# Optimization experiments

Measured on AMD Instinct MI355X. Metric: run time of the kernel, lower is better.

The kernel has to match this reference:

```python
import jax, jax.numpy as jnp
import numpy as np

FEATURE_DIM = 768
LAMBDA_REG = 0.01
NUM_ITERS = 5
LR = 0.1
SIGMA = 2.0
MARGIN = 1.0
BN_EPS = 1e-5


def setup_inputs() -> dict:
    key = jax.random.key(0)
    ks = jax.random.split(key, 10)
    B, D = 32, FEATURE_DIM
    search_features = jax.random.normal(ks[0], (B, D, 32, 32), dtype=jnp.float32)
    target_features = jax.random.normal(ks[1], (B, D, 16, 16), dtype=jnp.float32)
    target_mask = jax.random.uniform(ks[2], (B, 1, 16, 16), dtype=jnp.float32)
    conv_w = jax.random.normal(ks[3], (D, D), dtype=jnp.float32) * (1.0 / np.sqrt(D))
    conv_b = jax.random.normal(ks[4], (D,), dtype=jnp.float32) * 0.01
    bn_gamma = jnp.ones((D,), dtype=jnp.float32)
    bn_beta = jnp.zeros((D,), dtype=jnp.float32)
    bn_mean = jax.random.normal(ks[5], (D,), dtype=jnp.float32) * 0.01
    bn_var = jax.random.uniform(ks[6], (D,), dtype=jnp.float32, minval=0.5, maxval=1.5)
    filter_init = jax.random.normal(ks[7], (1, D, 1, 1), dtype=jnp.float32) * 0.01
    return {
        "search_features": search_features,
        "target_features": target_features,
        "target_mask": target_mask,
        "conv_w": conv_w,
        "conv_b": conv_b,
        "bn_gamma": bn_gamma,
        "bn_beta": bn_beta,
        "bn_mean": bn_mean,
        "bn_var": bn_var,
        "filter_init": filter_init,
    }


def _proj(x, conv_w, conv_b, bn_gamma, bn_beta, bn_mean, bn_var):
    # 1x1 conv == channel-wise GEMM, then BatchNorm (eval mode, running stats)
    y = jnp.einsum('bdhw,ed->behw', x, conv_w) + conv_b[None, :, None, None]
    inv_std = bn_gamma / jnp.sqrt(bn_var + BN_EPS)
    return (y - bn_mean[None, :, None, None]) * inv_std[None, :, None, None] + bn_beta[None, :, None, None]


def _gaussian_label(mask):
    B, _, H, W = mask.shape
    yy, xx = jnp.meshgrid(jnp.arange(H, dtype=jnp.float32), jnp.arange(W, dtype=jnp.float32), indexing='ij')
    yy = yy[None, None]  # (1,1,H,W)
    xx = xx[None, None]
    msum = jnp.clip(mask.sum(axis=(2, 3), keepdims=True), 1.0)
    cy = (mask * yy).sum(axis=(2, 3), keepdims=True) / msum
    cx = (mask * xx).sum(axis=(2, 3), keepdims=True) / msum
    return jnp.exp(-((xx - cx) ** 2 + (yy - cy) ** 2) / (2.0 * SIGMA ** 2))


def reference(search_features, target_features, target_mask, conv_w, conv_b,
              bn_gamma, bn_beta, bn_mean, bn_var, filter_init):
    sp = _proj(search_features, conv_w, conv_b, bn_gamma, bn_beta, bn_mean, bn_var)
    tp = _proj(target_features, conv_w, conv_b, bn_gamma, bn_beta, bn_mean, bn_var)
    B = tp.shape[0]
    label = _gaussian_label(target_mask)  # (B,1,H',W')
    f = jnp.broadcast_to(filter_init, (B,) + filter_init.shape[1:])  # (B,D,1,1)
    for _ in range(NUM_ITERS):
        response = (tp * f).sum(axis=1, keepdims=True)  # (B,1,H',W')
        loss = jnp.maximum(MARGIN - response * label, 0.0)
        grad = jnp.where(loss > 0, -label * target_mask, 0.0)
        grad = grad.mean(axis=(2, 3), keepdims=True)  # (B,1,1,1), broadcasts over D
        f = f - LR * (grad + LAMBDA_REG * f)
    return (sp * f).sum(axis=1, keepdims=True)  # (B,1,H,W)
```

## Files before the change

### kernel.cpp

```cpp
#include <hip/hip_runtime.h>
#include <math.h>

#define DD   768
#define BB   32
#define NTP  256
#define NSP  1024
#define NT   (BB*NTP)
#define NS   (BB*NSP)
#define ECH  48
#define CHE  (DD/ECH)

#define OFF_UP  0
#define OFF_VP  (OFF_UP + ECH*DD)
#define OFF_U   (OFF_VP + ECH*DD)
#define OFF_V   (OFF_U + DD)
#define OFF_K   (OFF_V + DD)
#define OFF_C5  (OFF_K + 16)
#define OFF_TR0 (OFF_C5 + 48)
#define OFF_TS0 (OFF_TR0 + NT)

#define A5 0.99500999000499900f

__global__ void k_prep(const float* __restrict__ w, const float* __restrict__ cb,
                       const float* __restrict__ gamma, const float* __restrict__ beta,
                       const float* __restrict__ mean, const float* __restrict__ var,
                       const float* __restrict__ fi, float* __restrict__ ws) {
    int bx = blockIdx.x;
    int t = threadIdx.x;
    if (bx < ECH) {
        __shared__ float wu[CHE], wv[CHE];
        if (t < CHE) {
            int e = bx * CHE + t;
            float inv = gamma[e] / sqrtf(var[e] + 1e-5f);
            wv[t] = inv;
            wu[t] = inv * fi[e];
        }
        __syncthreads();
        if (t < 192) {
            const float4* w4 = (const float4*)w;
            float4 Ru = {0,0,0,0}, Rv = {0,0,0,0};
            #pragma unroll
            for (int j = 0; j < CHE; ++j) {
                float4 x = w4[(size_t)(bx * CHE + j) * 192 + t];
                float a = wu[j], b = wv[j];
                Ru.x += x.x * a; Ru.y += x.y * a; Ru.z += x.z * a; Ru.w += x.w * a;
                Rv.x += x.x * b; Rv.y += x.y * b; Rv.z += x.z * b; Rv.w += x.w * b;
            }
            *(float4*)(ws + OFF_UP + bx * DD + t * 4) = Ru;
            *(float4*)(ws + OFF_VP + bx * DD + t * 4) = Rv;
        }
    } else {
        __shared__ float r1[256], r2[256];
        float a1 = 0.f, a2 = 0.f;
        for (int e = t; e < DD; e += 256) {
            float inv = gamma[e] / sqrtf(var[e] + 1e-5f);
            float x = (cb[e] - mean[e]) * inv + beta[e];
            a1 += x * fi[e];
            a2 += x;
        }
        r1[t] = a1; r2[t] = a2;
        __syncthreads();
        for (int s = 128; s > 0; s >>= 1) {
            if (t < s) { r1[t] += r1[t + s]; r2[t] += r2[t + s]; }
            __syncthreads();
        }
        if (t == 0) { ws[OFF_K] = r1[0]; ws[OFF_K + 1] = r2[0]; }
    }
}

__global__ void k_prep2(float* __restrict__ ws) {
    int bx = blockIdx.x;
    int d = (bx % 3) * 256 + threadIdx.x;
    int isV = bx / 3;
    int srcOff = isV ? OFF_VP : OFF_UP;
    int dstOff = isV ? OFF_V : OFF_U;
    float a = 0.f;
    #pragma unroll 8
    for (int ec = 0; ec < ECH; ++ec) a += ws[srcOff + ec * DD + d];
    ws[dstOff + d] = a;
}

__global__ __launch_bounds__(256) void k_dots_t(const float* __restrict__ tf,
                                                float* __restrict__ ws) {
    int t = threadIdx.x;
    int px = t & 15, sub = t >> 4;
    __shared__ float su[DD], sv[DD];
    for (int i = t; i < DD; i += 256) { su[i] = ws[OFF_U + i]; sv[i] = ws[OFF_V + i]; }
    __syncthreads();
    int pf = blockIdx.x * 16 + px;
    int b = pf >> 6;
    const float4* base = (const float4*)tf + ((size_t)b * DD + sub * 48) * (NTP/4) + (pf & 63);
    const int STR = NTP / 4;
    float4 accR = {0,0,0,0}, accS = {0,0,0,0};
    float4 buf[8];
    #pragma unroll
    for (int k = 0; k < 8; ++k) buf[k] = base[(size_t)k * STR];
    #pragma unroll
    for (int g = 1; g < 6; ++g) {
        float4 nxt[8];
        #pragma unroll
        for (int k = 0; k < 8; ++k) nxt[k] = base[(size_t)(g * 8 + k) * STR];
        #pragma unroll
        for (int k = 0; k < 8; ++k) {
            int ch = sub * 48 + (g - 1) * 8 + k;
            float u = su[ch], v = sv[ch];
            accR.x += buf[k].x * u; accR.y += buf[k].y * u; accR.z += buf[k].z * u; accR.w += buf[k].w * u;
            accS.x += buf[k].x * v; accS.y += buf[k].y * v; accS.z += buf[k].z * v; accS.w += buf[k].w * v;
            buf[k] = nxt[k];
        }
    }
    #pragma unroll
    for (int k = 0; k < 8; ++k) {
        int ch = sub * 48 + 40 + k;
        float u = su[ch], v = sv[ch];
        accR.x += buf[k].x * u; accR.y += buf[k].y * u; accR.z += buf[k].z * u; accR.w += buf[k].w * u;
        accS.x += buf[k].x * v; accS.y += buf[k].y * v; accS.z += buf[k].z * v; accS.w += buf[k].w * v;
    }
    __shared__ float4 redR[16][16], redS[16][16];
    redR[sub][px] = accR; redS[sub][px] = accS;
    __syncthreads();
    for (int s = 8; s > 0; s >>= 1) {
        if (sub < s) {
            float4 a = redR[sub + s][px], m = redR[sub][px];
            m.x += a.x; m.y += a.y; m.z += a.z; m.w += a.w; redR[sub][px] = m;
            float4 c = redS[sub + s][px], n = redS[sub][px];
            n.x += c.x; n.y += c.y; n.z += c.z; n.w += c.w; redS[sub][px] = n;
        }
        __syncthreads();
    }
    if (sub == 0) {
        ((float4*)(ws + OFF_TR0))[pf] = redR[0][px];
        ((float4*)(ws + OFF_TS0))[pf] = redS[0][px];
    }
}

__global__ void k_filter(const float* __restrict__ mask, float* __restrict__ ws) {
    int b = blockIdx.x;
    int p = threadIdx.x;
    int lane = p & 63, wv = p >> 6;
    int h = p >> 4, w = p & 15;
    float K1 = ws[OFF_K], K2 = ws[OFF_K + 1];
    float r0 = K1 + ws[OFF_TR0 + b * 256 + p];
    float s0 = K2 + ws[OFF_TS0 + b * 256 + p];
    float m = mask[b * 256 + p];
    __shared__ float cross[4];
    auto bsum = [&](float v) -> float {
        #pragma unroll
        for (int o = 32; o > 0; o >>= 1) v += __shfl_xor(v, o, 64);
        if (lane == 0) cross[wv] = v;
        __syncthreads();
        float r = cross[0] + cross[1] + cross[2] + cross[3];
        __syncthreads();
        return r;
    };
    float msum = bsum(m);
    float sy = bsum(m * (float)h);
    float sx = bsum(m * (float)w);
    msum = fmaxf(msum, 1.0f);
    float cy = sy / msum, cx = sx / msum;
    float dx = (float)w - cx, dy = (float)h - cy;
    float label = expf(-(dx * dx + dy * dy) * 0.125f);
    float A = 1.0f, c = 0.0f;
    const float decay = 1.0f - 0.1f * 0.01f;
    #pragma unroll
    for (int it = 0; it < 5; ++it) {
        float resp = A * r0 + c * s0;
        float gc = (1.0f - resp * label > 0.0f) ? (-label * m) : 0.0f;
        float g = bsum(gc) * (1.0f / 256.0f);
        c = decay * c - 0.1f * g;
        A *= decay;
    }
    if (p == 0) ws[OFF_C5 + b] = c;
}

__global__ __launch_bounds__(256) void k_out_s(const float* __restrict__ sf,
                                               const float* __restrict__ ws,
                                               float* __restrict__ out) {
    int t = threadIdx.x;
    int px = t & 15, sub = t >> 4;
    int pf = blockIdx.x * 16 + px;
    int b = pf >> 8;
    float c5 = ws[OFF_C5 + b];
    float K1 = ws[OFF_K], K2 = ws[OFF_K + 1];
    __shared__ float wc[DD];
    for (int i = t; i < DD; i += 256) wc[i] = A5 * ws[OFF_U + i] + c5 * ws[OFF_V + i];
    __syncthreads();
    const float4* base = (const float4*)sf + ((size_t)b * DD + sub * 48) * (NSP/4) + (pf & 255);
    const int STR = NSP / 4;
    float4 acc = {0,0,0,0};
    float4 buf[8];
    #pragma unroll
    for (int k = 0; k < 8; ++k) buf[k] = base[(size_t)k * STR];
    #pragma unroll
    for (int g = 1; g < 6; ++g) {
        float4 nxt[8];
        #pragma unroll
        for (int k = 0; k < 8; ++k) nxt[k] = base[(size_t)(g * 8 + k) * STR];
        #pragma unroll
        for (int k = 0; k < 8; ++k) {
            float u = wc[sub * 48 + (g - 1) * 8 + k];
            acc.x += buf[k].x * u; acc.y += buf[k].y * u; acc.z += buf[k].z * u; acc.w += buf[k].w * u;
            buf[k] = nxt[k];
        }
    }
    #pragma unroll
    for (int k = 0; k < 8; ++k) {
        float u = wc[sub * 48 + 40 + k];
        acc.x += buf[k].x * u; acc.y += buf[k].y * u; acc.z += buf[k].z * u; acc.w += buf[k].w * u;
    }
    __shared__ float4 red[16][16];
    red[sub][px] = acc;
    __syncthreads();
    for (int s = 8; s > 0; s >>= 1) {
        if (sub < s) {
            float4 a = red[sub + s][px], m = red[sub][px];
            m.x += a.x; m.y += a.y; m.z += a.z; m.w += a.w; red[sub][px] = m;
        }
        __syncthreads();
    }
    if (sub == 0) {
        float4 r = red[0][px];
        float kk = A5 * K1 + c5 * K2;
        r.x += kk; r.y += kk; r.z += kk; r.w += kk;
        ((float4*)out)[pf] = r;
    }
}

extern "C" void kernel_launch(void* const* d_in, const int* in_sizes, int n_in,
                              void* d_out, int out_size, void* d_ws, size_t ws_size,
                              hipStream_t stream) {
    const float* sf    = (const float*)d_in[0];
    const float* tf    = (const float*)d_in[1];
    const float* mask  = (const float*)d_in[2];
    const float* w     = (const float*)d_in[3];
    const float* cb    = (const float*)d_in[4];
    const float* gamma = (const float*)d_in[5];
    const float* beta  = (const float*)d_in[6];
    const float* mean  = (const float*)d_in[7];
    const float* var   = (const float*)d_in[8];
    const float* fi    = (const float*)d_in[9];
    float* out = (float*)d_out;
    float* ws  = (float*)d_ws;

    k_prep  <<<ECH + 1, 256, 0, stream>>>(w, cb, gamma, beta, mean, var, fi, ws);
    k_prep2 <<<6,       256, 0, stream>>>(ws);
    k_dots_t<<<128,     256, 0, stream>>>(tf, ws);
    k_filter<<<BB,      256, 0, stream>>>(mask, ws);
    k_out_s <<<512,     256, 0, stream>>>(sf, ws, out);
}
```

Measured before the change: 40.28 us.

## Compute search dots in parallel with target dots, apply filter coefficient in final pass

The output is linear in the filter coefficient, so the search-feature projections onto the two fixed vectors (u and v) are now computed in the same launch as the target dots. Previously they ran only after the per-batch filter solve. A combined kernel of 640 blocks handles search and target tiles, with a block-index remap that interleaves them. The final small kernel solves the filter and combines the two search partial sums per pixel. This removes one launch and the serialization of the large search read behind the filter step, at the cost of doubling FMAs on the search tensor and writing and reading two extra intermediate arrays.

```diff
diff --git a/kernel.cpp b/kernel.cpp
--- a/kernel.cpp
+++ b/kernel.cpp
@@ -15,9 +15,10 @@
 #define OFF_U   (OFF_VP + ECH*DD)
 #define OFF_V   (OFF_U + DD)
 #define OFF_K   (OFF_V + DD)
-#define OFF_C5  (OFF_K + 16)
-#define OFF_TR0 (OFF_C5 + 48)
+#define OFF_TR0 (OFF_K + 64)
 #define OFF_TS0 (OFF_TR0 + NT)
+#define OFF_SR  (OFF_TS0 + NT)
+#define OFF_SS  (OFF_SR + NS)
 
 #define A5 0.99500999000499900f
 
@@ -80,17 +81,35 @@
     ws[dstOff + d] = a;
 }
 
-__global__ __launch_bounds__(256) void k_dots_t(const float* __restrict__ tf,
-                                                float* __restrict__ ws) {
+__global__ __launch_bounds__(256) void k_big(const float* __restrict__ sf,
+                                             const float* __restrict__ tf,
+                                             float* __restrict__ ws) {
+    int bx = blockIdx.x;
+    int lb = (bx & 7) * 80 + (bx >> 3);
     int t = threadIdx.x;
     int px = t & 15, sub = t >> 4;
     __shared__ float su[DD], sv[DD];
     for (int i = t; i < DD; i += 256) { su[i] = ws[OFF_U + i]; sv[i] = ws[OFF_V + i]; }
     __syncthreads();
-    int pf = blockIdx.x * 16 + px;
-    int b = pf >> 6;
-    const float4* base = (const float4*)tf + ((size_t)b * DD + sub * 48) * (NTP/4) + (pf & 63);
-    const int STR = NTP / 4;
+
+    const float4* base;
+    int STR;
+    float4 *oR, *oS;
+    if (lb < 512) {
+        int pf = lb * 16 + px;
+        int b = pf >> 8;
+        base = (const float4*)sf + ((size_t)b * DD + sub * 48) * (NSP/4) + (pf & 255);
+        STR = NSP / 4;
+        oR = (float4*)(ws + OFF_SR) + pf;
+        oS = (float4*)(ws + OFF_SS) + pf;
+    } else {
+        int pf = (lb - 512) * 16 + px;
+        int b = pf >> 6;
+        base = (const float4*)tf + ((size_t)b * DD + sub * 48) * (NTP/4) + (pf & 63);
+        STR = NTP / 4;
+        oR = (float4*)(ws + OFF_TR0) + pf;
+        oS = (float4*)(ws + OFF_TS0) + pf;
+    }
     float4 accR = {0,0,0,0}, accS = {0,0,0,0};
     float4 buf[8];
     #pragma unroll
@@ -128,13 +147,11 @@
         }
         __syncthreads();
     }
-    if (sub == 0) {
-        ((float4*)(ws + OFF_TR0))[pf] = redR[0][px];
-        ((float4*)(ws + OFF_TS0))[pf] = redS[0][px];
-    }
-}
-
-__global__ void k_filter(const float* __restrict__ mask, float* __restrict__ ws) {
+    if (sub == 0) { *oR = redR[0][px]; *oS = redS[0][px]; }
+}
+
+__global__ void k_final(const float* __restrict__ mask, const float* __restrict__ ws,
+                        float* __restrict__ out) {
     int b = blockIdx.x;
     int p = threadIdx.x;
     int lane = p & 63, wv = p >> 6;
@@ -170,60 +187,15 @@
         c = decay * c - 0.1f * g;
         A *= decay;
     }
-    if (p == 0) ws[OFF_C5 + b] = c;
-}
-
-__global__ __launch_bounds__(256) void k_out_s(const float* __restrict__ sf,
-                                               const float* __restrict__ ws,
-                                               float* __restrict__ out) {
-    int t = threadIdx.x;
-    int px = t & 15, sub = t >> 4;
-    int pf = blockIdx.x * 16 + px;
-    int b = pf >> 8;
-    float c5 = ws[OFF_C5 + b];
-    float K1 = ws[OFF_K], K2 = ws[OFF_K + 1];
-    __shared__ float wc[DD];
-    for (int i = t; i < DD; i += 256) wc[i] = A5 * ws[OFF_U + i] + c5 * ws[OFF_V + i];
-    __syncthreads();
-    const float4* base = (const float4*)sf + ((size_t)b * DD + sub * 48) * (NSP/4) + (pf & 255);
-    const int STR = NSP / 4;
-    float4 acc = {0,0,0,0};
-    float4 buf[8];
-    #pragma unroll
-    for (int k = 0; k < 8; ++k) buf[k] = base[(size_t)k * STR];
-    #pragma unroll
-    for (int g = 1; g < 6; ++g) {
-        float4 nxt[8];
-        #pragma unroll
-        for (int k = 0; k < 8; ++k) nxt[k] = base[(size_t)(g * 8 + k) * STR];
-        #pragma unroll
-        for (int k = 0; k < 8; ++k) {
-            float u = wc[sub * 48 + (g - 1) * 8 + k];
-            acc.x += buf[k].x * u; acc.y += buf[k].y * u; acc.z += buf[k].z * u; acc.w += buf[k].w * u;
-            buf[k] = nxt[k];
-        }
-    }
-    #pragma unroll
-    for (int k = 0; k < 8; ++k) {
-        float u = wc[sub * 48 + 40 + k];
-        acc.x += buf[k].x * u; acc.y += buf[k].y * u; acc.z += buf[k].z * u; acc.w += buf[k].w * u;
-    }
-    __shared__ float4 red[16][16];
-    red[sub][px] = acc;
-    __syncthreads();
-    for (int s = 8; s > 0; s >>= 1) {
-        if (sub < s) {
-            float4 a = red[sub + s][px], m = red[sub][px];
-            m.x += a.x; m.y += a.y; m.z += a.z; m.w += a.w; red[sub][px] = m;
-        }
-        __syncthreads();
-    }
-    if (sub == 0) {
-        float4 r = red[0][px];
-        float kk = A5 * K1 + c5 * K2;
-        r.x += kk; r.y += kk; r.z += kk; r.w += kk;
-        ((float4*)out)[pf] = r;
-    }
+    int g4 = b * 256 + p;
+    float4 R = ((const float4*)(ws + OFF_SR))[g4];
+    float4 S = ((const float4*)(ws + OFF_SS))[g4];
+    float4 o;
+    o.x = A5 * (K1 + R.x) + c * (K2 + S.x);
+    o.y = A5 * (K1 + R.y) + c * (K2 + S.y);
+    o.z = A5 * (K1 + R.z) + c * (K2 + S.z);
+    o.w = A5 * (K1 + R.w) + c * (K2 + S.w);
+    ((float4*)out)[g4] = o;
 }
 
 extern "C" void kernel_launch(void* const* d_in, const int* in_sizes, int n_in,
@@ -242,9 +214,8 @@
     float* out = (float*)d_out;
     float* ws  = (float*)d_ws;
 
-    k_prep  <<<ECH + 1, 256, 0, stream>>>(w, cb, gamma, beta, mean, var, fi, ws);
-    k_prep2 <<<6,       256, 0, stream>>>(ws);
-    k_dots_t<<<128,     256, 0, stream>>>(tf, ws);
-    k_filter<<<BB,      256, 0, stream>>>(mask, ws);
-    k_out_s <<<512,     256, 0, stream>>>(sf, ws, out);
-}
+    k_prep <<<ECH + 1, 256, 0, stream>>>(w, cb, gamma, beta, mean, var, fi, ws);
+    k_prep2<<<6,       256, 0, stream>>>(ws);
+    k_big  <<<640,     256, 0, stream>>>(sf, tf, ws);
+    k_final<<<BB,      256, 0, stream>>>(mask, ws, out);
+}
```

New measurement: 38.34 us. -4.8%, faster.
